# Kernel optimization log

Hardware: AMD Instinct MI355X
Metric: run time of the kernel (lower is better)

## Reference

```python
import jax, jax.numpy as jnp
import numpy as np

B, T = 4, 2048          # batch, seq_len
D, H = 2048, 4096       # input_dim, router hidden_dim
E, O = 16, 2048         # num_experts, expert_output_dim
TAU = 0.5               # forward default tau


def setup_inputs() -> dict:
    key = jax.random.key(0)
    kx, k1, k2, k3, k4, k5, k6 = jax.random.split(key, 7)
    s = 0.02
    return {
        "x": jax.random.normal(kx, (B, T, D), dtype=jnp.float32),
        "W1": jax.random.normal(k1, (D, H), dtype=jnp.float32) * s,
        "b1": jnp.zeros((H,), dtype=jnp.float32),
        "W2": jax.random.normal(k2, (H, E), dtype=jnp.float32) * s,
        "b2": jnp.zeros((E,), dtype=jnp.float32),
        "We": jax.random.normal(k3, (E, D, O), dtype=jnp.float32) * s,
        "be": jnp.zeros((E, O), dtype=jnp.float32),
    }


def reference(x, W1, b1, W2, b2, We, be):
    # Router: Linear -> ReLU -> Linear -> softmax
    h = jax.nn.relu(jnp.einsum("btd,dh->bth", x, W1) + b1)
    logits = jnp.einsum("bth,he->bte", h, W2) + b2
    probs = jax.nn.softmax(logits, axis=-1)                 # [B,T,E]
    max_p = jnp.max(probs, axis=-1, keepdims=True)
    mask = probs >= TAU * max_p                              # [B,T,E] bool
    k_per_token = jnp.sum(mask, axis=-1)                     # [B,T] int
    gates = jnp.where(mask, probs, 0.0)                      # masked router probs
    # Per-expert dense Linear, masked weighted accumulate (E=16 is a fixed,
    # structurally distinct set; loop is over experts, not data dims).
    out = jnp.zeros((B, T, O), dtype=x.dtype)
    for i in range(E):
        expert_out = jnp.einsum("btd,do->bto", x, We[i]) + be[i]
        out = out + gates[..., i:i + 1] * expert_out
    return out, k_per_token
```

## Files before the change

### kernel.cpp

```cpp
#include <hip/hip_runtime.h>
#include <stdint.h>

#define M_TOK 8192
#define DDIM  2048
#define HDIM  4096
#define NEXP  16
#define ODIM  2048

typedef __attribute__((ext_vector_type(8))) __bf16 bf16x8;
typedef __attribute__((ext_vector_type(4))) float  f32x4;

__device__ __forceinline__ unsigned short f2bf(float f) {
    unsigned int u = __float_as_uint(f);
    unsigned int r = (u + 0x7FFFu + ((u >> 16) & 1u)) >> 16;
    return (unsigned short)r;
}
__device__ __forceinline__ float bf2f(unsigned short s) {
    return __uint_as_float(((unsigned int)s) << 16);
}


__global__ void split_x_kernel(const float* __restrict__ x,
                               ushort* __restrict__ xh, ushort* __restrict__ xl) {
    size_t i = ((size_t)blockIdx.x * 256 + threadIdx.x) * 4;
    float4 v = *(const float4*)(x + i);
    float f[4] = {v.x, v.y, v.z, v.w};
    ushort hu[4], lu[4];
#pragma unroll
    for (int u = 0; u < 4; ++u) {
        hu[u] = f2bf(f[u]);
        lu[u] = f2bf(f[u] - bf2f(hu[u]));
    }
    *(ushort4*)(xh + i) = make_ushort4(hu[0], hu[1], hu[2], hu[3]);
    *(ushort4*)(xl + i) = make_ushort4(lu[0], lu[1], lu[2], lu[3]);
}

__global__ void transpose_split_w1_kernel(const float* __restrict__ W1,
                                          ushort* __restrict__ th, ushort* __restrict__ tl) {
    __shared__ float tile[64][65];
    int h0 = (blockIdx.x & 63) * 64;
    int d0 = (blockIdx.x >> 6) * 64;
    int r = threadIdx.x >> 4;
    int c = (threadIdx.x & 15) * 4;
#pragma unroll
    for (int rr = 0; rr < 4; ++rr) {
        int row = rr * 16 + r;
        float4 v = *(const float4*)(W1 + (size_t)(d0 + row) * HDIM + h0 + c);
        tile[row][c + 0] = v.x; tile[row][c + 1] = v.y;
        tile[row][c + 2] = v.z; tile[row][c + 3] = v.w;
    }
    __syncthreads();
#pragma unroll
    for (int rr = 0; rr < 4; ++rr) {
        int hrow = rr * 16 + r;
        ushort hu[4], lu[4];
#pragma unroll
        for (int u = 0; u < 4; ++u) {
            float f = tile[c + u][hrow];
            hu[u] = f2bf(f);
            lu[u] = f2bf(f - bf2f(hu[u]));
        }
        size_t o = (size_t)(h0 + hrow) * DDIM + d0 + c;
        *(ushort4*)(th + o) = make_ushort4(hu[0], hu[1], hu[2], hu[3]);
        *(ushort4*)(tl + o) = make_ushort4(lu[0], lu[1], lu[2], lu[3]);
    }
}

__global__ void transpose_we_kernel(const float* __restrict__ We, ushort* __restrict__ wt) {
    __shared__ float tile[64][65];
    int e = blockIdx.y;
    int o0 = (blockIdx.x & 31) * 64;
    int d0 = (blockIdx.x >> 5) * 64;
    const float* src = We + (size_t)e * DDIM * ODIM;
    ushort* dst = wt + (size_t)e * ODIM * DDIM;
    int r = threadIdx.x >> 4;
    int c = (threadIdx.x & 15) * 4;
#pragma unroll
    for (int rr = 0; rr < 4; ++rr) {
        int row = rr * 16 + r;
        float4 v = *(const float4*)(src + (size_t)(d0 + row) * ODIM + o0 + c);
        tile[row][c + 0] = v.x; tile[row][c + 1] = v.y;
        tile[row][c + 2] = v.z; tile[row][c + 3] = v.w;
    }
    __syncthreads();
#pragma unroll
    for (int rr = 0; rr < 4; ++rr) {
        int orow = rr * 16 + r;
        ushort hu[4];
#pragma unroll
        for (int u = 0; u < 4; ++u) hu[u] = f2bf(tile[c + u][orow]);
        *(ushort4*)(dst + (size_t)(o0 + orow) * DDIM + d0 + c) =
            make_ushort4(hu[0], hu[1], hu[2], hu[3]);
    }
}


__device__ __forceinline__ void stage_tile(const ushort* __restrict__ g0, int ld,
                                           ushort* lds0, int wave, int lane) {
#pragma unroll
    for (int j = 0; j < 4; ++j) {
        int L = wave * 256 + j * 64 + lane;
        int m = L >> 3;
        int kc = (L & 7) ^ (m & 7);
        const ushort* gp = g0 + (size_t)m * ld + kc * 8;
        ushort* lp = lds0 + (size_t)(wave * 256 + j * 64) * 8;
        __builtin_amdgcn_global_load_lds(
            (const __attribute__((address_space(1))) void*)gp,
            (__attribute__((address_space(3))) void*)lp, 16, 0, 0);
    }
}

__device__ __forceinline__ bf16x8 ldfrag(const ushort* lds0, int row, int kc) {
    return *(const bf16x8*)(lds0 + ((row << 3) + (kc ^ (row & 7))) * 8);
}

__global__ __launch_bounds__(256, 2) void gemm1_kernel(
    const ushort* __restrict__ xh, const ushort* __restrict__ xl,
    const ushort* __restrict__ wh, const ushort* __restrict__ wl,
    const float* __restrict__ b1, float* __restrict__ hout) {
    __shared__ ushort As[8192];
    __shared__ ushort Bs[8192];
    const int tile_m = (blockIdx.x & 63) << 7;
    const int tile_n = (blockIdx.x >> 6) << 7;
    const int tid = threadIdx.x;
    const int wave = tid >> 6, lane = tid & 63;
    const int q = lane >> 4, mrow = lane & 15;
    const int wm = (wave >> 1) << 6, wn = (wave & 1) << 6;
    f32x4 acc[4][4];
#pragma unroll
    for (int i = 0; i < 4; ++i)
#pragma unroll
        for (int j = 0; j < 4; ++j) acc[i][j] = {0.f, 0.f, 0.f, 0.f};

    for (int it = 0; it < 96; ++it) {
        const int phase = it >> 5;
        const ushort* Ab = (phase == 1) ? xl : xh;
        const ushort* Bb = (phase == 2) ? wl : wh;
        const int k0 = (it & 31) << 6;
        __syncthreads();
        stage_tile(Ab + (size_t)tile_m * DDIM + k0, DDIM, As, wave, lane);
        stage_tile(Bb + (size_t)tile_n * DDIM + k0, DDIM, Bs, wave, lane);
        __syncthreads();
#pragma unroll
        for (int s = 0; s < 2; ++s) {
            bf16x8 af[4], bfr[4];
#pragma unroll
            for (int i = 0; i < 4; ++i) af[i] = ldfrag(As, wm + i * 16 + mrow, s * 4 + q);
#pragma unroll
            for (int j = 0; j < 4; ++j) bfr[j] = ldfrag(Bs, wn + j * 16 + mrow, s * 4 + q);
#pragma unroll
            for (int i = 0; i < 4; ++i)
#pragma unroll
                for (int j = 0; j < 4; ++j)
                    acc[i][j] = __builtin_amdgcn_mfma_f32_16x16x32_bf16(
                        af[i], bfr[j], acc[i][j], 0, 0, 0);
        }
    }
#pragma unroll
    for (int i = 0; i < 4; ++i) {
        const int r0 = tile_m + wm + i * 16 + q * 4;
#pragma unroll
        for (int j = 0; j < 4; ++j) {
            const int cc = tile_n + wn + j * 16 + mrow;
            const float bb = b1[cc];
#pragma unroll
            for (int r = 0; r < 4; ++r) {
                float v = acc[i][j][r] + bb;
                hout[(size_t)(r0 + r) * HDIM + cc] = v > 0.f ? v : 0.f;
            }
        }
    }
}

__global__ void gemm2_kernel(const float* __restrict__ h, const float* __restrict__ W2,
                             const float* __restrict__ b2, float* __restrict__ logits) {
    const int e = threadIdx.x & 15;
    const int t = blockIdx.x * 16 + (threadIdx.x >> 4);
    const float* hr = h + (size_t)t * HDIM;
    float acc = 0.f;
    for (int d = 0; d < HDIM; d += 8) {
#pragma unroll
        for (int u = 0; u < 8; ++u)
            acc = fmaf(hr[d + u], W2[(size_t)(d + u) * NEXP + e], acc);
    }
    logits[(size_t)t * NEXP + e] = acc + b2[e];
}

__global__ void gates_kernel(const float* __restrict__ logits,
                             float* __restrict__ gates, float* __restrict__ kout,
                             int* __restrict__ cnt, int* __restrict__ list) {
    const int t = blockIdx.x * 256 + threadIdx.x;
    float l[16];
    const float4* lp = (const float4*)(logits + (size_t)t * 16);
#pragma unroll
    for (int i = 0; i < 4; ++i) {
        float4 v = lp[i];
        l[i * 4] = v.x; l[i * 4 + 1] = v.y; l[i * 4 + 2] = v.z; l[i * 4 + 3] = v.w;
    }
    float lmax = l[0];
#pragma unroll
    for (int i = 1; i < 16; ++i) lmax = fmaxf(lmax, l[i]);
    float p[16], S = 0.f;
#pragma unroll
    for (int i = 0; i < 16; ++i) { p[i] = expf(l[i] - lmax); S += p[i]; }
#pragma unroll
    for (int i = 0; i < 16; ++i) p[i] /= S;
    float pmax = p[0];
#pragma unroll
    for (int i = 1; i < 16; ++i) pmax = fmaxf(pmax, p[i]);
    const float thr = 0.5f * pmax;
    int k = 0;
    float g[16];
#pragma unroll
    for (int i = 0; i < 16; ++i) {
        bool m = p[i] >= thr;
        g[i] = m ? p[i] : 0.f;
        k += m ? 1 : 0;
        if (m) {
            int pos = atomicAdd(&cnt[i], 1);
            list[i * M_TOK + pos] = t;
        }
    }
    float4* gp = (float4*)(gates + (size_t)t * 16);
#pragma unroll
    for (int i = 0; i < 4; ++i)
        gp[i] = make_float4(g[i * 4], g[i * 4 + 1], g[i * 4 + 2], g[i * 4 + 3]);
    kout[t] = (float)k;
}

__global__ void init_out_kernel(const float* __restrict__ gates,
                                const float* __restrict__ be, float* __restrict__ out) {
    const int t = blockIdx.x;
    const int tid = threadIdx.x;
    __shared__ float g[16];
    if (tid < 16) g[tid] = gates[(size_t)t * 16 + tid];
    __syncthreads();
    const int c0 = tid * 8;
    float a[8] = {0.f, 0.f, 0.f, 0.f, 0.f, 0.f, 0.f, 0.f};
#pragma unroll
    for (int e = 0; e < 16; ++e) {
        float ge = g[e];
        if (ge != 0.f) {
            float4 v1 = *(const float4*)(be + (size_t)e * ODIM + c0);
            float4 v2 = *(const float4*)(be + (size_t)e * ODIM + c0 + 4);
            a[0] = fmaf(ge, v1.x, a[0]); a[1] = fmaf(ge, v1.y, a[1]);
            a[2] = fmaf(ge, v1.z, a[2]); a[3] = fmaf(ge, v1.w, a[3]);
            a[4] = fmaf(ge, v2.x, a[4]); a[5] = fmaf(ge, v2.y, a[5]);
            a[6] = fmaf(ge, v2.z, a[6]); a[7] = fmaf(ge, v2.w, a[7]);
        }
    }
    *(float4*)(out + (size_t)t * ODIM + c0)     = make_float4(a[0], a[1], a[2], a[3]);
    *(float4*)(out + (size_t)t * ODIM + c0 + 4) = make_float4(a[4], a[5], a[6], a[7]);
}

__global__ __launch_bounds__(256, 3) void moe_sparse_kernel(
    const ushort* __restrict__ xh, const ushort* __restrict__ weT,
    const float* __restrict__ gates, const int* __restrict__ cnt,
    const int* __restrict__ list, float* __restrict__ out) {
    const int bx = blockIdx.x;
    const int e = bx >> 10;
    const int chunk = (bx >> 4) & 63;
    const int ntile = bx & 15;
    const int ce = cnt[e];
    const int row0 = chunk << 7;
    if (row0 >= ce) return;
    const int rows = min(128, ce - row0);

    __shared__ ushort As[8192];
    __shared__ ushort Bs[8192];
    __shared__ int toks[128];
    __shared__ float gv[128];

    const int tid = threadIdx.x;
    if (tid < 128) {
        int t = list[e * M_TOK + row0 + min(tid, rows - 1)];
        toks[tid] = t;
        gv[tid] = gates[(size_t)t * NEXP + e];
    }
    __syncthreads();

    const int wave = tid >> 6, lane = tid & 63;
    const int q = lane >> 4, mrow = lane & 15;
    const int wm = (wave >> 1) << 6, wn = (wave & 1) << 6;

    const ushort* agp[4];
    const ushort* bgp[4];
    ushort* alp[4];
    ushort* blp[4];
    const ushort* wbase = weT + ((size_t)e * ODIM + (ntile << 7)) * DDIM;
#pragma unroll
    for (int j = 0; j < 4; ++j) {
        int L = wave * 256 + j * 64 + lane;
        int m = L >> 3;
        int kc = (L & 7) ^ (m & 7);
        agp[j] = xh + (size_t)toks[m] * DDIM + kc * 8;
        bgp[j] = wbase + (size_t)m * DDIM + kc * 8;
        alp[j] = As + (size_t)L * 8;
        blp[j] = Bs + (size_t)L * 8;
    }

    f32x4 acc[4][4];
#pragma unroll
    for (int i = 0; i < 4; ++i)
#pragma unroll
        for (int j = 0; j < 4; ++j) acc[i][j] = {0.f, 0.f, 0.f, 0.f};

    for (int it = 0; it < 32; ++it) {
        const int k0 = it << 6;
        __syncthreads();
#pragma unroll
        for (int j = 0; j < 4; ++j) {
            __builtin_amdgcn_global_load_lds(
                (const __attribute__((address_space(1))) void*)(agp[j] + k0),
                (__attribute__((address_space(3))) void*)alp[j], 16, 0, 0);
            __builtin_amdgcn_global_load_lds(
                (const __attribute__((address_space(1))) void*)(bgp[j] + k0),
                (__attribute__((address_space(3))) void*)blp[j], 16, 0, 0);
        }
        __syncthreads();
#pragma unroll
        for (int s = 0; s < 2; ++s) {
            bf16x8 af[4], bfr[4];
#pragma unroll
            for (int i = 0; i < 4; ++i) af[i] = ldfrag(As, wm + i * 16 + mrow, s * 4 + q);
#pragma unroll
            for (int j = 0; j < 4; ++j) bfr[j] = ldfrag(Bs, wn + j * 16 + mrow, s * 4 + q);
#pragma unroll
            for (int i = 0; i < 4; ++i)
#pragma unroll
                for (int j = 0; j < 4; ++j)
                    acc[i][j] = __builtin_amdgcn_mfma_f32_16x16x32_bf16(
                        af[i], bfr[j], acc[i][j], 0, 0, 0);
        }
    }

#pragma unroll
    for (int i = 0; i < 4; ++i) {
        const int rl = wm + i * 16 + q * 4;
#pragma unroll
        for (int r = 0; r < 4; ++r) {
            const int lrow = rl + r;
            if (lrow < rows) {
                const int t = toks[lrow];
                const float g = gv[lrow];
                float* orow = out + (size_t)t * ODIM + (ntile << 7) + wn + mrow;
#pragma unroll
                for (int j = 0; j < 4; ++j)
                    atomicAdd(orow + j * 16, g * acc[i][j][r]);
            }
        }
    }
}

extern "C" void kernel_launch(void* const* d_in, const int* in_sizes, int n_in,
                              void* d_out, int out_size, void* d_ws, size_t ws_size,
                              hipStream_t stream) {
    const float* x  = (const float*)d_in[0];
    const float* W1 = (const float*)d_in[1];
    const float* b1 = (const float*)d_in[2];
    const float* W2 = (const float*)d_in[3];
    const float* b2 = (const float*)d_in[4];
    const float* We = (const float*)d_in[5];
    const float* be = (const float*)d_in[6];
    float* out  = (float*)d_out;
    float* kout = out + (size_t)M_TOK * ODIM;

    char* ws = (char*)d_ws;
    ushort* x_hi   = (ushort*)(ws);
    ushort* x_lo   = (ushort*)(ws + 33554432);
    ushort* w1t_hi = (ushort*)(ws + 67108864);
    ushort* w1t_lo = (ushort*)(ws + 83886080);
    int*    cnt    = (int*)   (ws + 83886080);
    int*    list   = (int*)   (ws + 83887104);
    float*  hbuf   = (float*) (ws + 100663296);
    ushort* weT    = (ushort*)(ws + 100663296);
    float*  logits = (float*) (ws + 234881024);
    float*  gates  = (float*) (ws + 235405312);

    split_x_kernel<<<16384, 256, 0, stream>>>(x, x_hi, x_lo);
    transpose_split_w1_kernel<<<2048, 256, 0, stream>>>(W1, w1t_hi, w1t_lo);
    gemm1_kernel<<<2048, 256, 0, stream>>>(x_hi, x_lo, w1t_hi, w1t_lo, b1, hbuf);
    gemm2_kernel<<<512, 256, 0, stream>>>(hbuf, W2, b2, logits);
    hipMemsetAsync(cnt, 0, 64, stream);
    gates_kernel<<<32, 256, 0, stream>>>(logits, gates, kout, cnt, list);
    dim3 gwe(1024, 16);
    transpose_we_kernel<<<gwe, 256, 0, stream>>>(We, weT);
    init_out_kernel<<<M_TOK, 256, 0, stream>>>(gates, be, out);
    moe_sparse_kernel<<<16384, 256, 0, stream>>>(x_hi, weT, gates, cnt, list, out);
}
```

Before: 1.314 ms.

## Fuse router second linear into gemm1 epilogue with atomic logit accumulation

The ReLU'd hidden tile is staged through shared memory inside gemm1 and immediately multiplied by the matching W2 rows, so each block produces partial logits that are atomically added into a zeroed buffer. This removes the 128MB fp32 hidden-activation write and reread along with the separate gemm2 kernel; the b2 bias moves into the gates kernel. In exchange it adds 32 atomics per token row and extra shared memory (33.5KB) in gemm1. Float atomics also make the logit summation order nondeterministic.

```diff
diff --git a/kernel.cpp b/kernel.cpp
--- a/kernel.cpp
+++ b/kernel.cpp
@@ -117,9 +117,13 @@
 __global__ __launch_bounds__(256, 2) void gemm1_kernel(
     const ushort* __restrict__ xh, const ushort* __restrict__ xl,
     const ushort* __restrict__ wh, const ushort* __restrict__ wl,
-    const float* __restrict__ b1, float* __restrict__ hout) {
-    __shared__ ushort As[8192];
-    __shared__ ushort Bs[8192];
+    const float* __restrict__ b1, const float* __restrict__ W2,
+    float* __restrict__ logits) {
+    __shared__ __align__(16) char smem_raw[33536];
+    ushort* As = (ushort*)smem_raw;
+    ushort* Bs = (ushort*)(smem_raw + 16384);
+    float*  hs = (float*)smem_raw;
+
     const int tile_m = (blockIdx.x & 63) << 7;
     const int tile_n = (blockIdx.x >> 6) << 7;
     const int tid = threadIdx.x;
@@ -156,37 +160,46 @@
                         af[i], bfr[j], acc[i][j], 0, 0, 0);
         }
     }
-#pragma unroll
-    for (int i = 0; i < 4; ++i) {
-        const int r0 = tile_m + wm + i * 16 + q * 4;
-#pragma unroll
-        for (int j = 0; j < 4; ++j) {
-            const int cc = tile_n + wn + j * 16 + mrow;
-            const float bb = b1[cc];
-#pragma unroll
-            for (int r = 0; r < 4; ++r) {
-                float v = acc[i][j][r] + bb;
-                hout[(size_t)(r0 + r) * HDIM + cc] = v > 0.f ? v : 0.f;
-            }
-        }
-    }
-}
-
-__global__ void gemm2_kernel(const float* __restrict__ h, const float* __restrict__ W2,
-                             const float* __restrict__ b2, float* __restrict__ logits) {
-    const int e = threadIdx.x & 15;
-    const int t = blockIdx.x * 16 + (threadIdx.x >> 4);
-    const float* hr = h + (size_t)t * HDIM;
-    float acc = 0.f;
-    for (int d = 0; d < HDIM; d += 8) {
-#pragma unroll
-        for (int u = 0; u < 8; ++u)
-            acc = fmaf(hr[d + u], W2[(size_t)(d + u) * NEXP + e], acc);
-    }
-    logits[(size_t)t * NEXP + e] = acc + b2[e];
-}
-
-__global__ void gates_kernel(const float* __restrict__ logits,
+
+    float part[8] = {0.f, 0.f, 0.f, 0.f, 0.f, 0.f, 0.f, 0.f};
+    const int prow = tid & 127;
+    const int e0 = (tid >> 7) << 3;
+#pragma unroll
+    for (int half = 0; half < 2; ++half) {
+        __syncthreads();
+        if (wn == (half << 6)) {
+#pragma unroll
+            for (int i = 0; i < 4; ++i)
+#pragma unroll
+                for (int j = 0; j < 4; ++j) {
+                    const int cc_l = j * 16 + mrow;
+                    const float bb = b1[tile_n + (half << 6) + cc_l];
+#pragma unroll
+                    for (int r = 0; r < 4; ++r) {
+                        float v = acc[i][j][r] + bb;
+                        hs[(wm + i * 16 + q * 4 + r) * 65 + cc_l] = v > 0.f ? v : 0.f;
+                    }
+                }
+        }
+        __syncthreads();
+        const float* W2h = W2 + ((size_t)(tile_n + (half << 6)) << 4) + e0;
+#pragma unroll 16
+        for (int c = 0; c < 64; ++c) {
+            const float hv = hs[prow * 65 + c];
+            const float4 wa = *(const float4*)(W2h + c * 16);
+            const float4 wb = *(const float4*)(W2h + c * 16 + 4);
+            part[0] = fmaf(hv, wa.x, part[0]); part[1] = fmaf(hv, wa.y, part[1]);
+            part[2] = fmaf(hv, wa.z, part[2]); part[3] = fmaf(hv, wa.w, part[3]);
+            part[4] = fmaf(hv, wb.x, part[4]); part[5] = fmaf(hv, wb.y, part[5]);
+            part[6] = fmaf(hv, wb.z, part[6]); part[7] = fmaf(hv, wb.w, part[7]);
+        }
+    }
+#pragma unroll
+    for (int u = 0; u < 8; ++u)
+        atomicAdd(&logits[((size_t)(tile_m + prow) << 4) + e0 + u], part[u]);
+}
+
+__global__ void gates_kernel(const float* __restrict__ logits, const float* __restrict__ b2,
                              float* __restrict__ gates, float* __restrict__ kout,
                              int* __restrict__ cnt, int* __restrict__ list) {
     const int t = blockIdx.x * 256 + threadIdx.x;
@@ -197,6 +210,8 @@
         float4 v = lp[i];
         l[i * 4] = v.x; l[i * 4 + 1] = v.y; l[i * 4 + 2] = v.z; l[i * 4 + 3] = v.w;
     }
+#pragma unroll
+    for (int i = 0; i < 16; ++i) l[i] += b2[i];
     float lmax = l[0];
 #pragma unroll
     for (int i = 1; i < 16; ++i) lmax = fmaxf(lmax, l[i]);
@@ -372,17 +387,16 @@
     ushort* w1t_lo = (ushort*)(ws + 83886080);
     int*    cnt    = (int*)   (ws + 83886080);
     int*    list   = (int*)   (ws + 83887104);
-    float*  hbuf   = (float*) (ws + 100663296);
     ushort* weT    = (ushort*)(ws + 100663296);
     float*  logits = (float*) (ws + 234881024);
     float*  gates  = (float*) (ws + 235405312);
 
     split_x_kernel<<<16384, 256, 0, stream>>>(x, x_hi, x_lo);
     transpose_split_w1_kernel<<<2048, 256, 0, stream>>>(W1, w1t_hi, w1t_lo);
-    gemm1_kernel<<<2048, 256, 0, stream>>>(x_hi, x_lo, w1t_hi, w1t_lo, b1, hbuf);
-    gemm2_kernel<<<512, 256, 0, stream>>>(hbuf, W2, b2, logits);
+    hipMemsetAsync(logits, 0, (size_t)M_TOK * NEXP * sizeof(float), stream);
     hipMemsetAsync(cnt, 0, 64, stream);
-    gates_kernel<<<32, 256, 0, stream>>>(logits, gates, kout, cnt, list);
+    gemm1_kernel<<<2048, 256, 0, stream>>>(x_hi, x_lo, w1t_hi, w1t_lo, b1, W2, logits);
+    gates_kernel<<<32, 256, 0, stream>>>(logits, b2, gates, kout, cnt, list);
     dim3 gwe(1024, 16);
     transpose_we_kernel<<<gwe, 256, 0, stream>>>(We, weT);
     init_out_kernel<<<M_TOK, 256, 0, stream>>>(gates, be, out);
```

Result: slower. 1.405 ms (+6.9%).
